# Performance work log

Hardware: AMD Instinct MI355X
Metric: run time of the kernel (lower is better)

The kernel has to match this reference:

```python
import jax, jax.numpy as jnp
import numpy as np

B, T, D = 1024, 12, 512


def setup_inputs() -> dict:
    key = jax.random.key(0)
    k1, k2 = jax.random.split(key)
    predictions = jax.random.normal(k1, (B, T, D), dtype=jnp.float32)
    x_future_encoded = jax.random.normal(k2, (B, T, D), dtype=jnp.float32)
    return {"predictions": predictions, "x_future_encoded": x_future_encoded}


def reference(predictions, x_future_encoded):
    # predictions, x_future_encoded: [B, T, D]
    b, t, _ = predictions.shape
    # dot[t, i, j] = <x_future_encoded[i, t], predictions[j, t]>  (matmul with transpose_b)
    dots = jnp.einsum('itd,jtd->tij', x_future_encoded, predictions)  # [T, B, B]
    # log_softmax over axis=0 of each [B, B] slice -> axis=1 of [T, B, B]
    log_sm = jax.nn.log_softmax(dots, axis=1)
    diag = jnp.diagonal(log_sm, axis1=1, axis2=2)          # [T, B]
    losses = jnp.sum(diag, axis=0) / t                      # [B]
    loss = jnp.mean(losses)
    # argmax of softmax(axis=0) == argmax of logits over axis=0
    pred_idx = jnp.argmax(dots, axis=1)                     # [T, B]
    correct = (pred_idx == jnp.arange(b)[None, :]).astype(jnp.float32)
    accuracy = jnp.mean(correct)  # == mean over t of count_nonzero/B
    return (-1.0 * loss, accuracy)
```

## Files before the change

kernel.cpp:

```cpp
#include <hip/hip_runtime.h>
#include <cstdint>
#include <cstddef>

#define Bsz 1024
#define Tsz 12
#define Dsz 512

#define BM 128
#define BN 128
#define BK 32
#define NIB (Bsz / BN)
#define NJB (Bsz / BM)
#define NKS (Dsz / BK)

typedef _Float16 f16x8 __attribute__((ext_vector_type(8)));
typedef float    f32x4 __attribute__((ext_vector_type(4)));

__device__ __forceinline__ f16x8 cvt8(const f32x4 v0, const f32x4 v1) {
    f16x8 h;
#pragma unroll
    for (int e = 0; e < 4; ++e) {
        h[e]     = (_Float16)v0[e];
        h[e + 4] = (_Float16)v1[e];
    }
    return h;
}

__global__ __launch_bounds__(256, 3) void gemm_fused_kernel(
    const float* __restrict__ P,
    const float* __restrict__ X,
    float* __restrict__ pm,
    float* __restrict__ ps,
    int*   __restrict__ pa,
    float* __restrict__ diag,
    float* __restrict__ out)
{
    const int orig = blockIdx.x + (blockIdx.y << 3) + (blockIdx.z << 6);
    const int wgid = (orig & 7) * 96 + (orig >> 3);
    const int t   = wgid >> 6;
    const int rem = wgid & 63;
    const int by  = rem >> 3;
    const int bx  = rem & 7;
    const int ib = bx * BN;
    const int jb = by * BM;

    const int tid  = threadIdx.x;
    const int lane = tid & 63;
    const int w    = tid >> 6;
    const int jw   = (w >> 1) * 64;
    const int iw   = (w & 1) * 64;
    const int ml   = lane & 15;
    const int quad = lane >> 4;

    if (orig == 0 && tid < 2) out[tid] = 0.0f;

    __shared__ _Float16 AH[2][BM][BK];
    __shared__ _Float16 BH[2][BN][BK];
    __shared__ float sm_m[BM][2];
    __shared__ float sm_s[BM][2];
    __shared__ int   sm_a[BM][2];

    f32x4 acc[4][4];
#pragma unroll
    for (int r = 0; r < 4; ++r)
#pragma unroll
        for (int c = 0; c < 4; ++c) acc[r][c] = (f32x4){0.f, 0.f, 0.f, 0.f};

    const int arr  = w >> 1;
    const int wsub = w & 1;
    const float* srcb = arr ? X : P;
    const int rb = (arr ? ib : jb) + wsub * 64;
    const int lrow = lane >> 2;
    const int g    = lane & 3;
    const int swl  = (lane >> 3) & 3;
    const size_t strideRow = (size_t)Tsz * Dsz;
    const float* gsrc = srcb + (size_t)(rb + lrow) * strideRow
                      + (size_t)t * Dsz + g * 8;
    _Float16* ldst = (arr ? &BH[0][0][0] : &AH[0][0][0])
                   + (wsub * 64 + lrow) * BK + ((g ^ swl) << 3);

    const int fsw = (quad ^ ((ml >> 1) & 3)) << 3;

    f32x4 ld[4][2];

#define ISSUE(k0f)                                                            \
    do {                                                                      \
        _Pragma("unroll")                                                     \
        for (int h_ = 0; h_ < 4; ++h_) {                                      \
            const float* s_ = gsrc + (size_t)h_ * 16 * strideRow + (k0f);     \
            ld[h_][0] = *(const f32x4*)(s_);                                  \
            ld[h_][1] = *(const f32x4*)(s_ + 4);                              \
        }                                                                     \
    } while (0)

#define WRITEB(bsel)                                                          \
    do {                                                                      \
        _Pragma("unroll")                                                     \
        for (int h_ = 0; h_ < 4; ++h_)                                        \
            *(f16x8*)(ldst + (bsel) * (BM * BK) + h_ * 16 * BK)               \
                = cvt8(ld[h_][0], ld[h_][1]);                                 \
    } while (0)

    ISSUE(0);
    WRITEB(0);
    __syncthreads();

    for (int ks = 0; ks < NKS; ++ks) {
        const int cur = ks & 1;
        if (ks + 1 < NKS) {
            ISSUE((ks + 1) * BK);
            __builtin_amdgcn_sched_barrier(0);
        }

        f16x8 ah[4], bh[4];
#pragma unroll
        for (int r = 0; r < 4; ++r)
            ah[r] = *(const f16x8*)&AH[cur][jw + r * 16 + ml][fsw];
#pragma unroll
        for (int c = 0; c < 4; ++c)
            bh[c] = *(const f16x8*)&BH[cur][iw + c * 16 + ml][fsw];

#pragma unroll
        for (int r = 0; r < 4; ++r)
#pragma unroll
            for (int c = 0; c < 4; ++c)
                acc[r][c] = __builtin_amdgcn_mfma_f32_16x16x32_f16(ah[r], bh[c], acc[r][c], 0, 0, 0);

        if (ks + 1 < NKS) WRITEB(cur ^ 1);
        __syncthreads();
    }
#undef ISSUE
#undef WRITEB

#pragma unroll
    for (int r = 0; r < 4; ++r)
#pragma unroll
        for (int v = 0; v < 4; ++v) {
            const int jg = jb + jw + r * 16 + quad * 4 + v;
#pragma unroll
            for (int c = 0; c < 4; ++c) {
                const int ig = ib + iw + c * 16 + ml;
                if (ig == jg) diag[(size_t)t * Bsz + jg] = acc[r][c][v];
            }
        }

#pragma unroll
    for (int r = 0; r < 4; ++r)
#pragma unroll
        for (int v = 0; v < 4; ++v) {
            float m = acc[r][0][v];
            int   ai = iw + ml;
#pragma unroll
            for (int c = 1; c < 4; ++c) {
                const float val = acc[r][c][v];
                if (val > m) { m = val; ai = iw + c * 16 + ml; }
            }
#pragma unroll
            for (int off = 1; off < 16; off <<= 1) {
                const float om = __shfl_xor(m, off);
                const int   oi = __shfl_xor(ai, off);
                if (om > m || (om == m && oi < ai)) { m = om; ai = oi; }
            }
            float s = 0.0f;
#pragma unroll
            for (int c = 0; c < 4; ++c) s += __expf(acc[r][c][v] - m);
#pragma unroll
            for (int off = 1; off < 16; off <<= 1) s += __shfl_xor(s, off);

            if (ml == 0) {
                const int row = jw + r * 16 + quad * 4 + v;
                sm_m[row][iw >> 6] = m;
                sm_s[row][iw >> 6] = s;
                sm_a[row][iw >> 6] = ib + ai;
            }
        }
    __syncthreads();

    if (tid < BM) {
        const int row = tid;
        const float m0 = sm_m[row][0], m1 = sm_m[row][1];
        const float s0 = sm_s[row][0], s1 = sm_s[row][1];
        float M; int A;
        if (m1 > m0) { M = m1; A = sm_a[row][1]; }
        else         { M = m0; A = sm_a[row][0]; }
        const float S = s0 * __expf(m0 - M) + s1 * __expf(m1 - M);
        const size_t slot = ((size_t)t * Bsz + (jb + row)) * NIB + bx;
        pm[slot] = M;
        ps[slot] = S;
        pa[slot] = A;
    }
}

__global__ __launch_bounds__(256) void combine_kernel(
    const float* __restrict__ pm,
    const float* __restrict__ ps,
    const int*   __restrict__ pa,
    const float* __restrict__ diag,
    float* __restrict__ out)
{
    const int col = blockIdx.x * 256 + threadIdx.x;
    const int j = col & (Bsz - 1);

    const size_t base = (size_t)col * NIB;
    float M = pm[base]; int A = pa[base];
#pragma unroll
    for (int b = 1; b < NIB; ++b) {
        const float mb = pm[base + b];
        if (mb > M) { M = mb; A = pa[base + b]; }
    }
    float S = 0.0f;
#pragma unroll
    for (int b = 0; b < NIB; ++b) S += ps[base + b] * __expf(pm[base + b] - M);

    const float lse = M + logf(S);
    float sl = lse - diag[col];
    float sc = (A == j) ? 1.0f : 0.0f;

#pragma unroll
    for (int off = 1; off < 64; off <<= 1) {
        sl += __shfl_xor(sl, off);
        sc += __shfl_xor(sc, off);
    }

    __shared__ float wl[4], wc[4];
    const int w = threadIdx.x >> 6;
    if ((threadIdx.x & 63) == 0) { wl[w] = sl; wc[w] = sc; }
    __syncthreads();
    if (threadIdx.x == 0) {
        const float inv = 1.0f / (float)(Bsz * Tsz);
        atomicAdd(&out[0], (wl[0] + wl[1] + wl[2] + wl[3]) * inv);
        atomicAdd(&out[1], (wc[0] + wc[1] + wc[2] + wc[3]) * inv);
    }
}

extern "C" void kernel_launch(void* const* d_in, const int* in_sizes, int n_in,
                              void* d_out, int out_size, void* d_ws, size_t ws_size,
                              hipStream_t stream) {
    const float* P = (const float*)d_in[0];
    const float* X = (const float*)d_in[1];
    float* out = (float*)d_out;

    const size_t ncol  = (size_t)Bsz * Tsz;
    const size_t nslot = ncol * NIB;

    float* pm   = (float*)d_ws;
    float* ps   = pm + nslot;
    int*   pa   = (int*)(ps + nslot);
    float* diag = (float*)(pa + nslot);

    gemm_fused_kernel<<<dim3(NIB, NJB, Tsz), dim3(256), 0, stream>>>(
        P, X, pm, ps, pa, diag, out);

    combine_kernel<<<dim3((int)(ncol / 256)), dim3(256), 0, stream>>>(
        pm, ps, pa, diag, out);
}
```

Measured before the change: 110.6 us.

## Pre-convert inputs to fp16 MFMA-fragment layout and drop LDS staging in GEMM

Adds a conversion kernel that writes both inputs as fp16 in a layout matching the MFMA fragments. The GEMM then loads its operands straight from global memory, with no LDS double buffering or barriers. It uses a 64x256 tile per workgroup, with each wave owning a 64x64 sub-tile and writing its partial max/sum/argmax directly. This doubles the partial slots to 16 per column. The cost is an extra kernel launch and an extra fp16 round-trip through memory, and each wave now re-reads the shared A strip from global or cache rather than sharing it through LDS.

```diff
diff --git a/kernel.cpp b/kernel.cpp
--- a/kernel.cpp
+++ b/kernel.cpp
@@ -6,12 +6,8 @@
 #define Tsz 12
 #define Dsz 512
 
-#define BM 128
-#define BN 128
-#define BK 32
-#define NIB (Bsz / BN)
-#define NJB (Bsz / BM)
-#define NKS (Dsz / BK)
+#define NIB 16
+#define NKS 16
 
 typedef _Float16 f16x8 __attribute__((ext_vector_type(8)));
 typedef float    f32x4 __attribute__((ext_vector_type(4)));
@@ -26,120 +22,94 @@
     return h;
 }
 
+__global__ __launch_bounds__(256) void convert_kernel(
+    const float* __restrict__ P, const float* __restrict__ X,
+    _Float16* __restrict__ Af, _Float16* __restrict__ Bf,
+    float* __restrict__ out)
+{
+    if (blockIdx.x == 0 && blockIdx.y == 0 && blockIdx.z == 0 && threadIdx.x < 2)
+        out[threadIdx.x] = 0.0f;
+
+    const int tid  = threadIdx.x;
+    const int w    = tid >> 6;
+    const int lane = tid & 63;
+    const int rb   = blockIdx.x >> 2;
+    const int ks   = ((blockIdx.x & 3) << 2) + w;
+    const int t    = blockIdx.y;
+    const int arr  = blockIdx.z;
+
+    const float* src = arr ? X : P;
+    _Float16*    dst = arr ? Bf : Af;
+
+    const int bl   = lane >> 2;
+    const int doct = lane & 3;
+    const float* s = src + ((size_t)(rb * 16 + bl) * Tsz + t) * Dsz
+                   + (size_t)ks * 32 + doct * 8;
+    const f32x4 v0 = *(const f32x4*)s;
+    const f32x4 v1 = *(const f32x4*)(s + 4);
+
+    const int lo = bl + (doct << 4);
+    _Float16* dp = dst + ((((size_t)t * 64 + rb) * 16 + ks) * 64 + lo) * 8;
+    *(f16x8*)dp = cvt8(v0, v1);
+}
+
 __global__ __launch_bounds__(256, 3) void gemm_fused_kernel(
-    const float* __restrict__ P,
-    const float* __restrict__ X,
+    const _Float16* __restrict__ Af,
+    const _Float16* __restrict__ Bf,
     float* __restrict__ pm,
     float* __restrict__ ps,
     int*   __restrict__ pa,
-    float* __restrict__ diag,
-    float* __restrict__ out)
+    float* __restrict__ diag)
 {
-    const int orig = blockIdx.x + (blockIdx.y << 3) + (blockIdx.z << 6);
+    const int orig = blockIdx.x + (blockIdx.y << 2) + (blockIdx.z << 6);
     const int wgid = (orig & 7) * 96 + (orig >> 3);
-    const int t   = wgid >> 6;
-    const int rem = wgid & 63;
-    const int by  = rem >> 3;
-    const int bx  = rem & 7;
-    const int ib = bx * BN;
-    const int jb = by * BM;
+    const int t      = wgid >> 6;
+    const int rem    = wgid & 63;
+    const int jstrip = rem >> 2;
+    const int ic     = rem & 3;
+    const int jb  = jstrip * 64;
 
     const int tid  = threadIdx.x;
     const int lane = tid & 63;
     const int w    = tid >> 6;
-    const int jw   = (w >> 1) * 64;
-    const int iw   = (w & 1) * 64;
+    const int ibw  = ic * 256 + w * 64;
     const int ml   = lane & 15;
     const int quad = lane >> 4;
 
-    if (orig == 0 && tid < 2) out[tid] = 0.0f;
-
-    __shared__ _Float16 AH[2][BM][BK];
-    __shared__ _Float16 BH[2][BN][BK];
-    __shared__ float sm_m[BM][2];
-    __shared__ float sm_s[BM][2];
-    __shared__ int   sm_a[BM][2];
-
     f32x4 acc[4][4];
 #pragma unroll
     for (int r = 0; r < 4; ++r)
 #pragma unroll
         for (int c = 0; c < 4; ++c) acc[r][c] = (f32x4){0.f, 0.f, 0.f, 0.f};
 
-    const int arr  = w >> 1;
-    const int wsub = w & 1;
-    const float* srcb = arr ? X : P;
-    const int rb = (arr ? ib : jb) + wsub * 64;
-    const int lrow = lane >> 2;
-    const int g    = lane & 3;
-    const int swl  = (lane >> 3) & 3;
-    const size_t strideRow = (size_t)Tsz * Dsz;
-    const float* gsrc = srcb + (size_t)(rb + lrow) * strideRow
-                      + (size_t)t * Dsz + g * 8;
-    _Float16* ldst = (arr ? &BH[0][0][0] : &AH[0][0][0])
-                   + (wsub * 64 + lrow) * BK + ((g ^ swl) << 3);
-
-    const int fsw = (quad ^ ((ml >> 1) & 3)) << 3;
-
-    f32x4 ld[4][2];
-
-#define ISSUE(k0f)                                                            \
-    do {                                                                      \
-        _Pragma("unroll")                                                     \
-        for (int h_ = 0; h_ < 4; ++h_) {                                      \
-            const float* s_ = gsrc + (size_t)h_ * 16 * strideRow + (k0f);     \
-            ld[h_][0] = *(const f32x4*)(s_);                                  \
-            ld[h_][1] = *(const f32x4*)(s_ + 4);                              \
-        }                                                                     \
-    } while (0)
-
-#define WRITEB(bsel)                                                          \
-    do {                                                                      \
-        _Pragma("unroll")                                                     \
-        for (int h_ = 0; h_ < 4; ++h_)                                        \
-            *(f16x8*)(ldst + (bsel) * (BM * BK) + h_ * 16 * BK)               \
-                = cvt8(ld[h_][0], ld[h_][1]);                                 \
-    } while (0)
-
-    ISSUE(0);
-    WRITEB(0);
-    __syncthreads();
-
+    const _Float16* Ap = Af + ((size_t)(t * 64 + (jb  >> 4)) * 16 * 64 + lane) * 8;
+    const _Float16* Bp = Bf + ((size_t)(t * 64 + (ibw >> 4)) * 16 * 64 + lane) * 8;
+
+#pragma unroll 4
     for (int ks = 0; ks < NKS; ++ks) {
-        const int cur = ks & 1;
-        if (ks + 1 < NKS) {
-            ISSUE((ks + 1) * BK);
-            __builtin_amdgcn_sched_barrier(0);
-        }
-
         f16x8 ah[4], bh[4];
 #pragma unroll
         for (int r = 0; r < 4; ++r)
-            ah[r] = *(const f16x8*)&AH[cur][jw + r * 16 + ml][fsw];
+            ah[r] = *(const f16x8*)(Ap + (size_t)(r * 16 + ks) * 512);
 #pragma unroll
         for (int c = 0; c < 4; ++c)
-            bh[c] = *(const f16x8*)&BH[cur][iw + c * 16 + ml][fsw];
+            bh[c] = *(const f16x8*)(Bp + (size_t)(c * 16 + ks) * 512);
 
 #pragma unroll
         for (int r = 0; r < 4; ++r)
 #pragma unroll
             for (int c = 0; c < 4; ++c)
                 acc[r][c] = __builtin_amdgcn_mfma_f32_16x16x32_f16(ah[r], bh[c], acc[r][c], 0, 0, 0);
-
-        if (ks + 1 < NKS) WRITEB(cur ^ 1);
-        __syncthreads();
-    }
-#undef ISSUE
-#undef WRITEB
+    }
 
 #pragma unroll
     for (int r = 0; r < 4; ++r)
 #pragma unroll
         for (int v = 0; v < 4; ++v) {
-            const int jg = jb + jw + r * 16 + quad * 4 + v;
+            const int jg = jb + r * 16 + quad * 4 + v;
 #pragma unroll
             for (int c = 0; c < 4; ++c) {
-                const int ig = ib + iw + c * 16 + ml;
+                const int ig = ibw + c * 16 + ml;
                 if (ig == jg) diag[(size_t)t * Bsz + jg] = acc[r][c][v];
             }
         }
@@ -149,11 +119,11 @@
 #pragma unroll
         for (int v = 0; v < 4; ++v) {
             float m = acc[r][0][v];
-            int   ai = iw + ml;
+            int   ai = ml;
 #pragma unroll
             for (int c = 1; c < 4; ++c) {
                 const float val = acc[r][c][v];
-                if (val > m) { m = val; ai = iw + c * 16 + ml; }
+                if (val > m) { m = val; ai = c * 16 + ml; }
             }
 #pragma unroll
             for (int off = 1; off < 16; off <<= 1) {
@@ -168,27 +138,13 @@
             for (int off = 1; off < 16; off <<= 1) s += __shfl_xor(s, off);
 
             if (ml == 0) {
-                const int row = jw + r * 16 + quad * 4 + v;
-                sm_m[row][iw >> 6] = m;
-                sm_s[row][iw >> 6] = s;
-                sm_a[row][iw >> 6] = ib + ai;
+                const int row = jb + r * 16 + quad * 4 + v;
+                const size_t slot = ((size_t)t * Bsz + row) * NIB + (ibw >> 6);
+                pm[slot] = m;
+                ps[slot] = s;
+                pa[slot] = ibw + ai;
             }
         }
-    __syncthreads();
-
-    if (tid < BM) {
-        const int row = tid;
-        const float m0 = sm_m[row][0], m1 = sm_m[row][1];
-        const float s0 = sm_s[row][0], s1 = sm_s[row][1];
-        float M; int A;
-        if (m1 > m0) { M = m1; A = sm_a[row][1]; }
-        else         { M = m0; A = sm_a[row][0]; }
-        const float S = s0 * __expf(m0 - M) + s1 * __expf(m1 - M);
-        const size_t slot = ((size_t)t * Bsz + (jb + row)) * NIB + bx;
-        pm[slot] = M;
-        ps[slot] = S;
-        pa[slot] = A;
-    }
 }
 
 __global__ __launch_bounds__(256) void combine_kernel(
@@ -242,14 +198,19 @@
 
     const size_t ncol  = (size_t)Bsz * Tsz;
     const size_t nslot = ncol * NIB;
+    const size_t nel   = (size_t)Bsz * Tsz * Dsz;
 
     float* pm   = (float*)d_ws;
     float* ps   = pm + nslot;
     int*   pa   = (int*)(ps + nslot);
     float* diag = (float*)(pa + nslot);
-
-    gemm_fused_kernel<<<dim3(NIB, NJB, Tsz), dim3(256), 0, stream>>>(
-        P, X, pm, ps, pa, diag, out);
+    _Float16* Af = (_Float16*)(diag + ncol);
+    _Float16* Bf = Af + nel;
+
+    convert_kernel<<<dim3(256, Tsz, 2), dim3(256), 0, stream>>>(P, X, Af, Bf, out);
+
+    gemm_fused_kernel<<<dim3(4, 16, Tsz), dim3(256), 0, stream>>>(
+        Af, Bf, pm, ps, pa, diag);
 
     combine_kernel<<<dim3((int)(ncol / 256)), dim3(256), 0, stream>>>(
         pm, ps, pa, diag, out);
```

New measurement: 115.1 us. 1.04x slower.

## Deepen global load prefetch to two stages with double register buffers

Applied to the files above, without the earlier changes.

Adds a second register staging buffer so global loads are issued two K-steps ahead instead of one, and unrolls the main loop by two with the LDS buffer indices fixed at compile time. The aim is to hide more global memory latency behind the MFMA work. In exchange, register pressure rises by 32 floats per thread, which may hurt occupancy under launch_bounds(256,3).

```diff
diff --git a/kernel.cpp b/kernel.cpp
--- a/kernel.cpp
+++ b/kernel.cpp
@@ -81,9 +81,9 @@
 
     const int fsw = (quad ^ ((ml >> 1) & 3)) << 3;
 
-    f32x4 ld[4][2];
-
-#define ISSUE(k0f)                                                            \
+    f32x4 ldA[4][2], ldB[4][2];
+
+#define ISSUE(ld, k0f)                                                        \
     do {                                                                      \
         _Pragma("unroll")                                                     \
         for (int h_ = 0; h_ < 4; ++h_) {                                      \
@@ -93,7 +93,7 @@
         }                                                                     \
     } while (0)
 
-#define WRITEB(bsel)                                                          \
+#define WRITEB(bsel, ld)                                                      \
     do {                                                                      \
         _Pragma("unroll")                                                     \
         for (int h_ = 0; h_ < 4; ++h_)                                        \
@@ -101,36 +101,47 @@
                 = cvt8(ld[h_][0], ld[h_][1]);                                 \
     } while (0)
 
-    ISSUE(0);
-    WRITEB(0);
-    __syncthreads();
-
-    for (int ks = 0; ks < NKS; ++ks) {
-        const int cur = ks & 1;
-        if (ks + 1 < NKS) {
-            ISSUE((ks + 1) * BK);
-            __builtin_amdgcn_sched_barrier(0);
-        }
-
-        f16x8 ah[4], bh[4];
-#pragma unroll
-        for (int r = 0; r < 4; ++r)
-            ah[r] = *(const f16x8*)&AH[cur][jw + r * 16 + ml][fsw];
-#pragma unroll
-        for (int c = 0; c < 4; ++c)
-            bh[c] = *(const f16x8*)&BH[cur][iw + c * 16 + ml][fsw];
-
-#pragma unroll
-        for (int r = 0; r < 4; ++r)
-#pragma unroll
-            for (int c = 0; c < 4; ++c)
-                acc[r][c] = __builtin_amdgcn_mfma_f32_16x16x32_f16(ah[r], bh[c], acc[r][c], 0, 0, 0);
-
-        if (ks + 1 < NKS) WRITEB(cur ^ 1);
+#define COMPUTE(bsel)                                                         \
+    do {                                                                      \
+        f16x8 ah[4], bh[4];                                                   \
+        _Pragma("unroll")                                                     \
+        for (int r_ = 0; r_ < 4; ++r_)                                        \
+            ah[r_] = *(const f16x8*)&AH[bsel][jw + r_ * 16 + ml][fsw];        \
+        _Pragma("unroll")                                                     \
+        for (int c_ = 0; c_ < 4; ++c_)                                        \
+            bh[c_] = *(const f16x8*)&BH[bsel][iw + c_ * 16 + ml][fsw];        \
+        _Pragma("unroll")                                                     \
+        for (int r_ = 0; r_ < 4; ++r_)                                        \
+            _Pragma("unroll")                                                 \
+            for (int c_ = 0; c_ < 4; ++c_)                                    \
+                acc[r_][c_] = __builtin_amdgcn_mfma_f32_16x16x32_f16(         \
+                    ah[r_], bh[c_], acc[r_][c_], 0, 0, 0);                    \
+    } while (0)
+
+    ISSUE(ldA, 0);
+    WRITEB(0, ldA);
+    ISSUE(ldB, BK);
+    __syncthreads();
+
+    for (int k2 = 0; k2 < NKS - 2; k2 += 2) {
+        ISSUE(ldA, (k2 + 2) * BK);
+        __builtin_amdgcn_sched_barrier(0);
+        COMPUTE(0);
+        WRITEB(1, ldB);
         __syncthreads();
-    }
+        ISSUE(ldB, (k2 + 3) * BK);
+        __builtin_amdgcn_sched_barrier(0);
+        COMPUTE(1);
+        WRITEB(0, ldA);
+        __syncthreads();
+    }
+    COMPUTE(0);
+    WRITEB(1, ldB);
+    __syncthreads();
+    COMPUTE(1);
 #undef ISSUE
 #undef WRITEB
+#undef COMPUTE
 
 #pragma unroll
     for (int r = 0; r < 4; ++r)
```

After: 135.6 us. +22.6%, slower.

## Shrink GEMM tile to 128x64, unify LDS buffer, raise occupancy to 5 waves

Applied to the files above, without the earlier changes.

The i-dimension tile drops from 128 to 64, so the grid doubles to 1536 workgroups. Each wave now holds a 4x2 MFMA accumulator instead of 4x4, and launch bounds ask for 5 waves per SIMD instead of 3. The A and B shared tiles merge into one 192-row buffer, and the softmax reduction scratch reuses that buffer to cut LDS per block. In exchange, operand reuse per block falls, P rows are loaded twice as often, and the combine kernel must reduce 16 partials per column instead of 8.

```diff
diff --git a/kernel.cpp b/kernel.cpp
--- a/kernel.cpp
+++ b/kernel.cpp
@@ -6,12 +6,13 @@
 #define Tsz 12
 #define Dsz 512
 
-#define BM 128
-#define BN 128
-#define BK 32
-#define NIB (Bsz / BN)
-#define NJB (Bsz / BM)
+#define BMJ 128
+#define BNI 64
+#define BK  32
+#define NIB (Bsz / BNI)
+#define NJB (Bsz / BMJ)
 #define NKS (Dsz / BK)
+#define NWG (NIB * NJB * Tsz)
 
 typedef _Float16 f16x8 __attribute__((ext_vector_type(8)));
 typedef float    f32x4 __attribute__((ext_vector_type(4)));
@@ -26,7 +27,7 @@
     return h;
 }
 
-__global__ __launch_bounds__(256, 3) void gemm_fused_kernel(
+__global__ __launch_bounds__(256, 5) void gemm_fused_kernel(
     const float* __restrict__ P,
     const float* __restrict__ X,
     float* __restrict__ pm,
@@ -35,70 +36,69 @@
     float* __restrict__ diag,
     float* __restrict__ out)
 {
-    const int orig = blockIdx.x + (blockIdx.y << 3) + (blockIdx.z << 6);
-    const int wgid = (orig & 7) * 96 + (orig >> 3);
-    const int t   = wgid >> 6;
-    const int rem = wgid & 63;
-    const int by  = rem >> 3;
-    const int bx  = rem & 7;
-    const int ib = bx * BN;
-    const int jb = by * BM;
+    const int orig = blockIdx.x + (blockIdx.y << 4) + (blockIdx.z << 7);
+    const int wgid = (orig & 7) * (NWG / 8) + (orig >> 3);
+    const int t   = wgid >> 7;
+    const int rem = wgid & 127;
+    const int by  = rem >> 4;
+    const int bx  = rem & 15;
+    const int jb = by * BMJ;
+    const int ib = bx * BNI;
 
     const int tid  = threadIdx.x;
     const int lane = tid & 63;
     const int w    = tid >> 6;
-    const int jw   = (w >> 1) * 64;
-    const int iw   = (w & 1) * 64;
+    const int jw   = (w & 1) * 64;
+    const int iwl  = (w >> 1) * 32;
     const int ml   = lane & 15;
     const int quad = lane >> 4;
 
     if (orig == 0 && tid < 2) out[tid] = 0.0f;
 
-    __shared__ _Float16 AH[2][BM][BK];
-    __shared__ _Float16 BH[2][BN][BK];
-    __shared__ float sm_m[BM][2];
-    __shared__ float sm_s[BM][2];
-    __shared__ int   sm_a[BM][2];
-
-    f32x4 acc[4][4];
+    __shared__ _Float16 L[2][192][BK];
+    float* sm_m = (float*)&L[0][0][0];
+    float* sm_s = sm_m + 256;
+    int*   sm_a = (int*)(sm_s + 256);
+
+    f32x4 acc[4][2];
 #pragma unroll
     for (int r = 0; r < 4; ++r)
 #pragma unroll
-        for (int c = 0; c < 4; ++c) acc[r][c] = (f32x4){0.f, 0.f, 0.f, 0.f};
-
-    const int arr  = w >> 1;
-    const int wsub = w & 1;
-    const float* srcb = arr ? X : P;
-    const int rb = (arr ? ib : jb) + wsub * 64;
-    const int lrow = lane >> 2;
-    const int g    = lane & 3;
-    const int swl  = (lane >> 3) & 3;
+        for (int c = 0; c < 2; ++c) acc[r][c] = (f32x4){0.f, 0.f, 0.f, 0.f};
+
     const size_t strideRow = (size_t)Tsz * Dsz;
-    const float* gsrc = srcb + (size_t)(rb + lrow) * strideRow
-                      + (size_t)t * Dsz + g * 8;
-    _Float16* ldst = (arr ? &BH[0][0][0] : &AH[0][0][0])
-                   + (wsub * 64 + lrow) * BK + ((g ^ swl) << 3);
+    const int g  = lane & 3;
+    const int qb = w * 48 + (lane >> 2);
+    const float* gs[3];
+    int ldso[3];
+#pragma unroll
+    for (int h = 0; h < 3; ++h) {
+        const int q = qb + h * 16;
+        const float* base = (q < 128)
+            ? (P + (size_t)(jb + q) * strideRow)
+            : (X + (size_t)(ib + q - 128) * strideRow);
+        gs[h]   = base + (size_t)t * Dsz + g * 8;
+        ldso[h] = q * BK + ((g ^ ((q >> 1) & 3)) << 3);
+    }
 
     const int fsw = (quad ^ ((ml >> 1) & 3)) << 3;
 
-    f32x4 ld[4][2];
+    f32x4 ld[3][2];
 
 #define ISSUE(k0f)                                                            \
     do {                                                                      \
         _Pragma("unroll")                                                     \
-        for (int h_ = 0; h_ < 4; ++h_) {                                      \
-            const float* s_ = gsrc + (size_t)h_ * 16 * strideRow + (k0f);     \
-            ld[h_][0] = *(const f32x4*)(s_);                                  \
-            ld[h_][1] = *(const f32x4*)(s_ + 4);                              \
+        for (int h_ = 0; h_ < 3; ++h_) {                                      \
+            ld[h_][0] = *(const f32x4*)(gs[h_] + (k0f));                      \
+            ld[h_][1] = *(const f32x4*)(gs[h_] + (k0f) + 4);                  \
         }                                                                     \
     } while (0)
 
 #define WRITEB(bsel)                                                          \
     do {                                                                      \
         _Pragma("unroll")                                                     \
-        for (int h_ = 0; h_ < 4; ++h_)                                        \
-            *(f16x8*)(ldst + (bsel) * (BM * BK) + h_ * 16 * BK)               \
-                = cvt8(ld[h_][0], ld[h_][1]);                                 \
+        for (int h_ = 0; h_ < 3; ++h_)                                        \
+            *(f16x8*)(&L[bsel][0][0] + ldso[h_]) = cvt8(ld[h_][0], ld[h_][1]); \
     } while (0)
 
     ISSUE(0);
@@ -112,18 +112,18 @@
             __builtin_amdgcn_sched_barrier(0);
         }
 
-        f16x8 ah[4], bh[4];
+        f16x8 ah[4], bh[2];
 #pragma unroll
         for (int r = 0; r < 4; ++r)
-            ah[r] = *(const f16x8*)&AH[cur][jw + r * 16 + ml][fsw];
-#pragma unroll
-        for (int c = 0; c < 4; ++c)
-            bh[c] = *(const f16x8*)&BH[cur][iw + c * 16 + ml][fsw];
+            ah[r] = *(const f16x8*)&L[cur][jw + r * 16 + ml][fsw];
+#pragma unroll
+        for (int c = 0; c < 2; ++c)
+            bh[c] = *(const f16x8*)&L[cur][128 + iwl + c * 16 + ml][fsw];
 
 #pragma unroll
         for (int r = 0; r < 4; ++r)
 #pragma unroll
-            for (int c = 0; c < 4; ++c)
+            for (int c = 0; c < 2; ++c)
                 acc[r][c] = __builtin_amdgcn_mfma_f32_16x16x32_f16(ah[r], bh[c], acc[r][c], 0, 0, 0);
 
         if (ks + 1 < NKS) WRITEB(cur ^ 1);
@@ -138,8 +138,8 @@
         for (int v = 0; v < 4; ++v) {
             const int jg = jb + jw + r * 16 + quad * 4 + v;
 #pragma unroll
-            for (int c = 0; c < 4; ++c) {
-                const int ig = ib + iw + c * 16 + ml;
+            for (int c = 0; c < 2; ++c) {
+                const int ig = ib + iwl + c * 16 + ml;
                 if (ig == jg) diag[(size_t)t * Bsz + jg] = acc[r][c][v];
             }
         }
@@ -149,11 +149,10 @@
 #pragma unroll
         for (int v = 0; v < 4; ++v) {
             float m = acc[r][0][v];
-            int   ai = iw + ml;
-#pragma unroll
-            for (int c = 1; c < 4; ++c) {
-                const float val = acc[r][c][v];
-                if (val > m) { m = val; ai = iw + c * 16 + ml; }
+            int   ai = iwl + ml;
+            {
+                const float val = acc[r][1][v];
+                if (val > m) { m = val; ai = iwl + 16 + ml; }
             }
 #pragma unroll
             for (int off = 1; off < 16; off <<= 1) {
@@ -161,28 +160,27 @@
                 const int   oi = __shfl_xor(ai, off);
                 if (om > m || (om == m && oi < ai)) { m = om; ai = oi; }
             }
-            float s = 0.0f;
-#pragma unroll
-            for (int c = 0; c < 4; ++c) s += __expf(acc[r][c][v] - m);
+            float s = __expf(acc[r][0][v] - m) + __expf(acc[r][1][v] - m);
 #pragma unroll
             for (int off = 1; off < 16; off <<= 1) s += __shfl_xor(s, off);
 
             if (ml == 0) {
-                const int row = jw + r * 16 + quad * 4 + v;
-                sm_m[row][iw >> 6] = m;
-                sm_s[row][iw >> 6] = s;
-                sm_a[row][iw >> 6] = ib + ai;
+                const int row  = jw + r * 16 + quad * 4 + v;
+                const int half = iwl >> 5;
+                sm_m[row * 2 + half] = m;
+                sm_s[row * 2 + half] = s;
+                sm_a[row * 2 + half] = ib + ai;
             }
         }
     __syncthreads();
 
-    if (tid < BM) {
+    if (tid < BMJ) {
         const int row = tid;
-        const float m0 = sm_m[row][0], m1 = sm_m[row][1];
-        const float s0 = sm_s[row][0], s1 = sm_s[row][1];
+        const float m0 = sm_m[row * 2 + 0], m1 = sm_m[row * 2 + 1];
+        const float s0 = sm_s[row * 2 + 0], s1 = sm_s[row * 2 + 1];
         float M; int A;
-        if (m1 > m0) { M = m1; A = sm_a[row][1]; }
-        else         { M = m0; A = sm_a[row][0]; }
+        if (m1 > m0) { M = m1; A = sm_a[row * 2 + 1]; }
+        else         { M = m0; A = sm_a[row * 2 + 0]; }
         const float S = s0 * __expf(m0 - M) + s1 * __expf(m1 - M);
         const size_t slot = ((size_t)t * Bsz + (jb + row)) * NIB + bx;
         pm[slot] = M;
```

Result: slower. 120.5 us (+9.0%).
